# Performance work log

Measured on AMD Instinct MI355X. Metric: run time of the kernel, lower is better.

Reference implementation:

```python
import jax, jax.numpy as jnp
import numpy as np

D_MODEL = 256
N = 8192

def setup_inputs() -> dict:
    key = jax.random.key(0)
    k1, k2, k3, k4 = jax.random.split(key, 4)
    x = jax.random.normal(k1, (N, D_MODEL), dtype=jnp.float32)
    # nn.Linear weights: shape [out, in], applied as x @ W.T
    s = 1.0 / np.sqrt(D_MODEL)
    Wq = jax.random.normal(k2, (D_MODEL, D_MODEL), dtype=jnp.float32) * s
    Wk = jax.random.normal(k3, (D_MODEL, D_MODEL), dtype=jnp.float32) * s
    Wv = jax.random.normal(k4, (D_MODEL, D_MODEL), dtype=jnp.float32) * s
    return {"x": x, "Wq": Wq, "Wk": Wk, "Wv": Wv}

def reference(x, Wq, Wk, Wv):
    d_model = Wq.shape[0]
    Q = x @ Wq.T  # [N, d]
    K = x @ Wk.T
    V = x @ Wv.T
    scores = (Q @ K.T) / jnp.sqrt(jnp.asarray(d_model, x.dtype))  # [N, N]
    attn = jax.nn.softmax(scores, axis=-1)  # stable max-sub softmax, same math
    cntx = attn @ V  # [N, d]
    return (cntx, attn)
```

## Files before the change

kernel.cpp:

```cpp
#include <hip/hip_runtime.h>

#define D_MODEL 256
#define NSEQ    8192
#define PV_GROUPS 8

typedef _Float16 half8 __attribute__((ext_vector_type(8)));
typedef _Float16 half4 __attribute__((ext_vector_type(4)));
typedef float    f32x4 __attribute__((ext_vector_type(4)));

__device__ __forceinline__ half8 cvt8(f32x4 a, f32x4 b) {
  half8 h;
  h[0]=(_Float16)a[0]; h[1]=(_Float16)a[1]; h[2]=(_Float16)a[2]; h[3]=(_Float16)a[3];
  h[4]=(_Float16)b[0]; h[5]=(_Float16)b[1]; h[6]=(_Float16)b[2]; h[7]=(_Float16)b[3];
  return h;
}

__device__ __forceinline__ half8 load8_f32(const float* p) {
  f32x4 a = *(const f32x4*)p;
  f32x4 b = *(const f32x4*)(p + 4);
  return cvt8(a, b);
}

__global__ __launch_bounds__(64, 3) void qkv_kernel(
    const float* __restrict__ x, const float* __restrict__ Wq,
    const float* __restrict__ Wk, const float* __restrict__ Wv,
    _Float16* __restrict__ QK16, _Float16* __restrict__ VT)
{
  const int lane = threadIdx.x & 63;
  const int c    = lane & 15;
  const int quad = lane >> 4;
  const int M0   = blockIdx.x * 64;
  const int Nblk = blockIdx.y * 64;
  const int widx = Nblk >> 8;
  const int nloc = Nblk & 255;
  const float* W = (widx == 0) ? Wq : (widx == 1 ? Wk : Wv);

  f32x4 acc[4][4] = {};
  for (int k0 = 0; k0 < D_MODEL; k0 += 32) {
    half8 af[4], bf[4];
#pragma unroll
    for (int mt = 0; mt < 4; ++mt)
      af[mt] = load8_f32(&x[(size_t)(M0 + mt*16 + c) * D_MODEL + k0 + quad*8]);
#pragma unroll
    for (int nt = 0; nt < 4; ++nt)
      bf[nt] = load8_f32(&W[(size_t)(nloc + nt*16 + c) * D_MODEL + k0 + quad*8]);
#pragma unroll
    for (int mt = 0; mt < 4; ++mt)
#pragma unroll
      for (int nt = 0; nt < 4; ++nt)
        acc[mt][nt] = __builtin_amdgcn_mfma_f32_16x16x32_f16(af[mt], bf[nt], acc[mt][nt], 0, 0, 0);
  }

  if (widx < 2) {
#pragma unroll
    for (int mt = 0; mt < 4; ++mt)
#pragma unroll
      for (int nt = 0; nt < 4; ++nt) {
        const int col  = widx * 256 + nloc + nt*16 + c;
        const int row0 = M0 + mt*16 + quad*4;
#pragma unroll
        for (int r = 0; r < 4; ++r)
          QK16[(size_t)(row0 + r) * 512 + col] = (_Float16)acc[mt][nt][r];
      }
  } else {
#pragma unroll
    for (int mt = 0; mt < 4; ++mt)
#pragma unroll
      for (int nt = 0; nt < 4; ++nt) {
        const int d  = nloc + nt*16 + c;
        const int m0 = M0 + mt*16 + quad*4;
        half4 h;
        h[0]=(_Float16)acc[mt][nt][0]; h[1]=(_Float16)acc[mt][nt][1];
        h[2]=(_Float16)acc[mt][nt][2]; h[3]=(_Float16)acc[mt][nt][3];
        *(half4*)&VT[(size_t)d * NSEQ + m0] = h;
      }
  }
}

template<bool P16>
__global__ __launch_bounds__(256, 3) void score_kernel(
    const _Float16* __restrict__ QK16, void* __restrict__ Pout,
    float* __restrict__ lsum)
{
  const int tid  = threadIdx.x;
  const int lane = tid & 63;
  const int wave = tid >> 6;
  const int c    = lane & 15;
  const int quad = lane >> 4;
  const int M0   = blockIdx.x * 128 + (wave >> 1) * 64;
  const int N0   = blockIdx.y * 128 + (wave & 1) * 64;

  f32x4 acc[4][4] = {};
  half8 afA[4], bfA[4], afB[4], bfB[4];

  auto ld = [&](half8 (&af)[4], half8 (&bf)[4], int k0) {
#pragma unroll
    for (int mt = 0; mt < 4; ++mt)
      af[mt] = *(const half8*)&QK16[(size_t)(M0 + mt*16 + c) * 512 + k0 + quad*8];
#pragma unroll
    for (int nt = 0; nt < 4; ++nt)
      bf[nt] = *(const half8*)&QK16[(size_t)(N0 + nt*16 + c) * 512 + 256 + k0 + quad*8];
  };
  auto mm = [&](half8 (&af)[4], half8 (&bf)[4]) {
#pragma unroll
    for (int mt = 0; mt < 4; ++mt)
#pragma unroll
      for (int nt = 0; nt < 4; ++nt)
        acc[mt][nt] = __builtin_amdgcn_mfma_f32_16x16x32_f16(af[mt], bf[nt], acc[mt][nt], 0, 0, 0);
  };

  ld(afA, bfA, 0);
#pragma unroll
  for (int k0 = 0; k0 < 256; k0 += 64) {
    ld(afB, bfB, k0 + 32);
    mm(afA, bfA);
    if (k0 + 64 < 256) ld(afA, bfA, k0 + 64);
    mm(afB, bfB);
  }

  float psum[4][4] = {};
#pragma unroll
  for (int mt = 0; mt < 4; ++mt)
#pragma unroll
    for (int nt = 0; nt < 4; ++nt)
#pragma unroll
      for (int r = 0; r < 4; ++r) {
        const float p = __expf(acc[mt][nt][r] * 0.0625f);
        psum[mt][r] += p;
        const size_t idx = (size_t)(M0 + mt*16 + quad*4 + r) * NSEQ + N0 + nt*16 + c;
        if constexpr (P16) ((_Float16*)Pout)[idx] = (_Float16)p;
        else               ((float*)Pout)[idx]    = p;
      }

#pragma unroll
  for (int mt = 0; mt < 4; ++mt)
#pragma unroll
    for (int r = 0; r < 4; ++r) {
      float v = psum[mt][r];
      v += __shfl_xor(v, 1);
      v += __shfl_xor(v, 2);
      v += __shfl_xor(v, 4);
      v += __shfl_xor(v, 8);
      if (c == 0) atomicAdd(&lsum[M0 + mt*16 + quad*4 + r], v);
    }
}

__global__ __launch_bounds__(256, 3) void pv_kernel_p16(
    const _Float16* __restrict__ P16, float* __restrict__ attn,
    const float* __restrict__ lsum, const _Float16* __restrict__ VT,
    float* __restrict__ cntx)
{
  __shared__ float linv[32];
  const int tid  = threadIdx.x;
  const int lane = tid & 63;
  const int wave = tid >> 6;
  const int c    = lane & 15;
  const int quad = lane >> 4;
  const int M0   = blockIdx.x * 32;
  const int jb   = blockIdx.y * (NSEQ / PV_GROUPS);
  const int je   = jb + NSEQ / PV_GROUPS;
  const int D0   = wave * 64;
  const int nr   = tid >> 3;
  const int ncol = (tid & 7) * 8;

  if (tid < 32) linv[tid] = 1.0f / lsum[M0 + tid];
  __syncthreads();
  const float nscale = linv[nr];

  f32x4 acc[2][4] = {};
  half8 afA[2][2], bfA[4][2], npA;
  half8 afB[2][2], bfB[4][2], npB;

  auto ld = [&](half8 (&af)[2][2], half8 (&bf)[4][2], half8& np, int j0) {
    np = *(const half8*)&P16[(size_t)(M0 + nr) * NSEQ + j0 + ncol];
#pragma unroll
    for (int h = 0; h < 2; ++h) {
#pragma unroll
      for (int mt = 0; mt < 2; ++mt)
        af[mt][h] = *(const half8*)&P16[(size_t)(M0 + mt*16 + c) * NSEQ + j0 + h*32 + quad*8];
#pragma unroll
      for (int nt = 0; nt < 4; ++nt)
        bf[nt][h] = *(const half8*)&VT[(size_t)(D0 + nt*16 + c) * NSEQ + j0 + h*32 + quad*8];
    }
  };
  auto consume = [&](half8 (&af)[2][2], half8 (&bf)[4][2], half8& np, int j0) {
    f32x4 w0, w1;
#pragma unroll
    for (int r = 0; r < 4; ++r) {
      w0[r] = (float)np[r]     * nscale;
      w1[r] = (float)np[r + 4] * nscale;
    }
    float* ar = attn + (size_t)(M0 + nr) * NSEQ + j0 + ncol;
    *(f32x4*)ar       = w0;
    *(f32x4*)(ar + 4) = w1;
#pragma unroll
    for (int h = 0; h < 2; ++h)
#pragma unroll
      for (int mt = 0; mt < 2; ++mt)
#pragma unroll
        for (int nt = 0; nt < 4; ++nt)
          acc[mt][nt] = __builtin_amdgcn_mfma_f32_16x16x32_f16(af[mt][h], bf[nt][h], acc[mt][nt], 0, 0, 0);
  };

  ld(afA, bfA, npA, jb);
  for (int j0 = jb; j0 < je; j0 += 128) {
    ld(afB, bfB, npB, j0 + 64);
    consume(afA, bfA, npA, j0);
    if (j0 + 128 < je) ld(afA, bfA, npA, j0 + 128);
    consume(afB, bfB, npB, j0 + 64);
  }

#pragma unroll
  for (int mt = 0; mt < 2; ++mt)
#pragma unroll
    for (int r = 0; r < 4; ++r) {
      const float s = linv[mt*16 + quad*4 + r];
#pragma unroll
      for (int nt = 0; nt < 4; ++nt)
        atomicAdd(&cntx[(size_t)(M0 + mt*16 + quad*4 + r) * D_MODEL + D0 + nt*16 + c],
                  acc[mt][nt][r] * s);
    }
}

__global__ __launch_bounds__(256) void pv_kernel_f32(
    const float* __restrict__ Pin, float* __restrict__ attn,
    const float* __restrict__ lsum, const _Float16* __restrict__ VT,
    float* __restrict__ cntx)
{
  __shared__ float linv[32];
  const int tid  = threadIdx.x;
  const int lane = tid & 63;
  const int wave = tid >> 6;
  const int c    = lane & 15;
  const int quad = lane >> 4;
  const int M0   = blockIdx.x * 32;
  const int jb   = blockIdx.y * (NSEQ / PV_GROUPS);
  const int je   = jb + NSEQ / PV_GROUPS;
  const int D0   = wave * 64;
  const int nr   = tid >> 3;
  const int ncol = (tid & 7) * 8;

  if (tid < 32) linv[tid] = 1.0f / lsum[M0 + tid];
  __syncthreads();
  const float nscale = linv[nr];

  f32x4 acc[2][4] = {};
  for (int j0 = jb; j0 < je; j0 += 64) {
    const float* pr = Pin + (size_t)(M0 + nr) * NSEQ + j0 + ncol;
    f32x4 np0 = *(const f32x4*)pr;
    f32x4 np1 = *(const f32x4*)(pr + 4);

    half8 af[2][2], bf[4][2];
#pragma unroll
    for (int h = 0; h < 2; ++h) {
#pragma unroll
      for (int mt = 0; mt < 2; ++mt) {
        const float* pa = Pin + (size_t)(M0 + mt*16 + c) * NSEQ + j0 + h*32 + quad*8;
        af[mt][h] = cvt8(*(const f32x4*)pa, *(const f32x4*)(pa + 4));
      }
#pragma unroll
      for (int nt = 0; nt < 4; ++nt)
        bf[nt][h] = *(const half8*)&VT[(size_t)(D0 + nt*16 + c) * NSEQ + j0 + h*32 + quad*8];
    }

    __syncthreads();

    float* ar = attn + (size_t)(M0 + nr) * NSEQ + j0 + ncol;
    *(f32x4*)ar       = np0 * nscale;
    *(f32x4*)(ar + 4) = np1 * nscale;

#pragma unroll
    for (int h = 0; h < 2; ++h)
#pragma unroll
      for (int mt = 0; mt < 2; ++mt)
#pragma unroll
        for (int nt = 0; nt < 4; ++nt)
          acc[mt][nt] = __builtin_amdgcn_mfma_f32_16x16x32_f16(af[mt][h], bf[nt][h], acc[mt][nt], 0, 0, 0);
  }

#pragma unroll
  for (int mt = 0; mt < 2; ++mt)
#pragma unroll
    for (int r = 0; r < 4; ++r) {
      const float s = linv[mt*16 + quad*4 + r];
#pragma unroll
      for (int nt = 0; nt < 4; ++nt)
        atomicAdd(&cntx[(size_t)(M0 + mt*16 + quad*4 + r) * D_MODEL + D0 + nt*16 + c],
                  acc[mt][nt][r] * s);
    }
}

extern "C" void kernel_launch(void* const* d_in, const int* in_sizes, int n_in,
                              void* d_out, int out_size, void* d_ws, size_t ws_size,
                              hipStream_t stream)
{
  const float* x  = (const float*)d_in[0];
  const float* Wq = (const float*)d_in[1];
  const float* Wk = (const float*)d_in[2];
  const float* Wv = (const float*)d_in[3];

  float* cntx = (float*)d_out;
  float* attn = cntx + (size_t)NSEQ * D_MODEL;

  _Float16* QK16 = (_Float16*)d_ws;
  _Float16* VT   = QK16 + (size_t)NSEQ * 512;
  float*    lsum = (float*)(VT + (size_t)D_MODEL * NSEQ);
  _Float16* P16  = (_Float16*)(lsum + NSEQ);

  const size_t base_bytes = (size_t)NSEQ*512*2 + (size_t)D_MODEL*NSEQ*2 + (size_t)NSEQ*4;
  const bool big_ws = ws_size >= base_bytes + (size_t)NSEQ * NSEQ * 2;

  hipMemsetAsync(cntx, 0, sizeof(float) * (size_t)NSEQ * D_MODEL, stream);
  hipMemsetAsync(lsum, 0, sizeof(float) * NSEQ, stream);

  qkv_kernel<<<dim3(128, 12), 64, 0, stream>>>(x, Wq, Wk, Wv, QK16, VT);

  if (big_ws) {
    score_kernel<true><<<dim3(64, 64), 256, 0, stream>>>(QK16, (void*)P16, lsum);
    pv_kernel_p16<<<dim3(NSEQ/32, PV_GROUPS), 256, 0, stream>>>(P16, attn, lsum, VT, cntx);
  } else {
    score_kernel<false><<<dim3(64, 64), 256, 0, stream>>>(QK16, (void*)attn, lsum);
    pv_kernel_f32<<<dim3(NSEQ/32, PV_GROUPS), 256, 0, stream>>>(attn, attn, lsum, VT, cntx);
  }
}
```

Before: 642.2 us.

## Store fp16 probabilities in MFMA-fragment tiled layout and stage via LDS DMA

```diff
diff --git a/kernel.cpp b/kernel.cpp
--- a/kernel.cpp
+++ b/kernel.cpp
@@ -7,6 +7,9 @@
 typedef _Float16 half8 __attribute__((ext_vector_type(8)));
 typedef _Float16 half4 __attribute__((ext_vector_type(4)));
 typedef float    f32x4 __attribute__((ext_vector_type(4)));
+
+typedef __attribute__((address_space(1))) const void* gptr_t;
+typedef __attribute__((address_space(3))) void*       lptr_t;
 
 __device__ __forceinline__ half8 cvt8(f32x4 a, f32x4 b) {
   half8 h;
@@ -20,6 +23,7 @@
   f32x4 b = *(const f32x4*)(p + 4);
   return cvt8(a, b);
 }
+
 
 __global__ __launch_bounds__(64, 3) void qkv_kernel(
     const float* __restrict__ x, const float* __restrict__ Wq,
@@ -120,17 +124,26 @@
 
   float psum[4][4] = {};
 #pragma unroll
-  for (int mt = 0; mt < 4; ++mt)
-#pragma unroll
-    for (int nt = 0; nt < 4; ++nt)
+  for (int mt = 0; mt < 4; ++mt) {
+    const size_t tq = (size_t)((M0 + mt*16) >> 4);
+#pragma unroll
+    for (int nt = 0; nt < 4; ++nt) {
+      const size_t tj   = (size_t)((N0 >> 5) + (nt >> 1));
+      const size_t base = (tq * 256 + tj) * 512
+                        + (size_t)(((nt*2 + (c>>3)) & 3) * 128 + quad*32 + (c & 7));
 #pragma unroll
       for (int r = 0; r < 4; ++r) {
         const float p = __expf(acc[mt][nt][r] * 0.0625f);
         psum[mt][r] += p;
-        const size_t idx = (size_t)(M0 + mt*16 + quad*4 + r) * NSEQ + N0 + nt*16 + c;
-        if constexpr (P16) ((_Float16*)Pout)[idx] = (_Float16)p;
-        else               ((float*)Pout)[idx]    = p;
-      }
+        if constexpr (P16) {
+          ((_Float16*)Pout)[base + r*8] = (_Float16)p;
+        } else {
+          const size_t idx = (size_t)(M0 + mt*16 + quad*4 + r) * NSEQ + N0 + nt*16 + c;
+          ((float*)Pout)[idx] = p;
+        }
+      }
+    }
+  }
 
 #pragma unroll
   for (int mt = 0; mt < 4; ++mt)
@@ -145,8 +158,99 @@
     }
 }
 
-__global__ __launch_bounds__(256, 3) void pv_kernel_p16(
-    const _Float16* __restrict__ P16, float* __restrict__ attn,
+__global__ __launch_bounds__(256) void pv_kernel_p16(
+    const _Float16* __restrict__ P16F, float* __restrict__ attn,
+    const float* __restrict__ lsum, const _Float16* __restrict__ VT,
+    float* __restrict__ cntx)
+{
+  __shared__ alignas(16) _Float16 As[2 * 4 * 512];
+  __shared__ float linv[32];
+  const int tid  = threadIdx.x;
+  const int lane = tid & 63;
+  const int wave = tid >> 6;
+  const int c    = lane & 15;
+  const int quad = lane >> 4;
+  const int M0   = blockIdx.x * 32;
+  const int jb   = blockIdx.y * (NSEQ / PV_GROUPS);
+  const int je   = jb + NSEQ / PV_GROUPS;
+  const int D0   = wave * 64;
+  const int wmt  = wave >> 1;
+  const int wks  = wave & 1;
+
+  if (tid < 32) linv[tid] = 1.0f / lsum[M0 + tid];
+
+  const size_t tq = (size_t)((M0 >> 4) + wmt);
+
+  {
+    const _Float16* src = P16F + (tq * 256 + (size_t)((jb >> 5) + wks)) * 512 + lane * 8;
+    __builtin_amdgcn_global_load_lds((gptr_t)src, (lptr_t)&As[wave * 512], 16, 0, 0);
+  }
+  __syncthreads();
+
+  const float sw = linv[wmt * 16 + c];
+
+  f32x4 acc[2][4] = {};
+  int buf = 0;
+  for (int j0 = jb; j0 < je; j0 += 64) {
+    if (j0 + 64 < je) {
+      const _Float16* src = P16F + (tq * 256 + (size_t)(((j0 + 64) >> 5) + wks)) * 512 + lane * 8;
+      __builtin_amdgcn_global_load_lds((gptr_t)src,
+          (lptr_t)&As[(buf ^ 1) * 2048 + wave * 512], 16, 0, 0);
+    }
+
+    half8 af[2][2];
+#pragma unroll
+    for (int mt = 0; mt < 2; ++mt)
+#pragma unroll
+      for (int ks = 0; ks < 2; ++ks)
+        af[mt][ks] = *(const half8*)&As[buf * 2048 + (mt*2 + ks) * 512 + lane * 8];
+
+    half8 bf[4][2];
+#pragma unroll
+    for (int ks = 0; ks < 2; ++ks)
+#pragma unroll
+      for (int nt = 0; nt < 4; ++nt)
+        bf[nt][ks] = *(const half8*)&VT[(size_t)(D0 + nt*16 + c) * NSEQ + j0 + ks*32 + quad*8];
+
+    {
+      const half8 v = af[wmt][wks];
+      f32x4 w0, w1;
+#pragma unroll
+      for (int r = 0; r < 4; ++r) {
+        w0[r] = (float)v[r]     * sw;
+        w1[r] = (float)v[r + 4] * sw;
+      }
+      float* ar = attn + (size_t)(M0 + wmt*16 + c) * NSEQ + j0 + wks*32 + quad*8;
+      *(f32x4*)ar       = w0;
+      *(f32x4*)(ar + 4) = w1;
+    }
+
+#pragma unroll
+    for (int ks = 0; ks < 2; ++ks)
+#pragma unroll
+      for (int mt = 0; mt < 2; ++mt)
+#pragma unroll
+        for (int nt = 0; nt < 4; ++nt)
+          acc[mt][nt] = __builtin_amdgcn_mfma_f32_16x16x32_f16(af[mt][ks], bf[nt][ks], acc[mt][nt], 0, 0, 0);
+
+    __syncthreads();
+    buf ^= 1;
+  }
+
+#pragma unroll
+  for (int mt = 0; mt < 2; ++mt)
+#pragma unroll
+    for (int r = 0; r < 4; ++r) {
+      const float s = linv[mt*16 + quad*4 + r];
+#pragma unroll
+      for (int nt = 0; nt < 4; ++nt)
+        atomicAdd(&cntx[(size_t)(M0 + mt*16 + quad*4 + r) * D_MODEL + D0 + nt*16 + c],
+                  acc[mt][nt][r] * s);
+    }
+}
+
+__global__ __launch_bounds__(256) void pv_kernel_f32(
+    const float* __restrict__ Pin, float* __restrict__ attn,
     const float* __restrict__ lsum, const _Float16* __restrict__ VT,
     float* __restrict__ cntx)
 {
@@ -168,83 +272,6 @@
   const float nscale = linv[nr];
 
   f32x4 acc[2][4] = {};
-  half8 afA[2][2], bfA[4][2], npA;
-  half8 afB[2][2], bfB[4][2], npB;
-
-  auto ld = [&](half8 (&af)[2][2], half8 (&bf)[4][2], half8& np, int j0) {
-    np = *(const half8*)&P16[(size_t)(M0 + nr) * NSEQ + j0 + ncol];
-#pragma unroll
-    for (int h = 0; h < 2; ++h) {
-#pragma unroll
-      for (int mt = 0; mt < 2; ++mt)
-        af[mt][h] = *(const half8*)&P16[(size_t)(M0 + mt*16 + c) * NSEQ + j0 + h*32 + quad*8];
-#pragma unroll
-      for (int nt = 0; nt < 4; ++nt)
-        bf[nt][h] = *(const half8*)&VT[(size_t)(D0 + nt*16 + c) * NSEQ + j0 + h*32 + quad*8];
-    }
-  };
-  auto consume = [&](half8 (&af)[2][2], half8 (&bf)[4][2], half8& np, int j0) {
-    f32x4 w0, w1;
-#pragma unroll
-    for (int r = 0; r < 4; ++r) {
-      w0[r] = (float)np[r]     * nscale;
-      w1[r] = (float)np[r + 4] * nscale;
-    }
-    float* ar = attn + (size_t)(M0 + nr) * NSEQ + j0 + ncol;
-    *(f32x4*)ar       = w0;
-    *(f32x4*)(ar + 4) = w1;
-#pragma unroll
-    for (int h = 0; h < 2; ++h)
-#pragma unroll
-      for (int mt = 0; mt < 2; ++mt)
-#pragma unroll
-        for (int nt = 0; nt < 4; ++nt)
-          acc[mt][nt] = __builtin_amdgcn_mfma_f32_16x16x32_f16(af[mt][h], bf[nt][h], acc[mt][nt], 0, 0, 0);
-  };
-
-  ld(afA, bfA, npA, jb);
-  for (int j0 = jb; j0 < je; j0 += 128) {
-    ld(afB, bfB, npB, j0 + 64);
-    consume(afA, bfA, npA, j0);
-    if (j0 + 128 < je) ld(afA, bfA, npA, j0 + 128);
-    consume(afB, bfB, npB, j0 + 64);
-  }
-
-#pragma unroll
-  for (int mt = 0; mt < 2; ++mt)
-#pragma unroll
-    for (int r = 0; r < 4; ++r) {
-      const float s = linv[mt*16 + quad*4 + r];
-#pragma unroll
-      for (int nt = 0; nt < 4; ++nt)
-        atomicAdd(&cntx[(size_t)(M0 + mt*16 + quad*4 + r) * D_MODEL + D0 + nt*16 + c],
-                  acc[mt][nt][r] * s);
-    }
-}
-
-__global__ __launch_bounds__(256) void pv_kernel_f32(
-    const float* __restrict__ Pin, float* __restrict__ attn,
-    const float* __restrict__ lsum, const _Float16* __restrict__ VT,
-    float* __restrict__ cntx)
-{
-  __shared__ float linv[32];
-  const int tid  = threadIdx.x;
-  const int lane = tid & 63;
-  const int wave = tid >> 6;
-  const int c    = lane & 15;
-  const int quad = lane >> 4;
-  const int M0   = blockIdx.x * 32;
-  const int jb   = blockIdx.y * (NSEQ / PV_GROUPS);
-  const int je   = jb + NSEQ / PV_GROUPS;
-  const int D0   = wave * 64;
-  const int nr   = tid >> 3;
-  const int ncol = (tid & 7) * 8;
-
-  if (tid < 32) linv[tid] = 1.0f / lsum[M0 + tid];
-  __syncthreads();
-  const float nscale = linv[nr];
-
-  f32x4 acc[2][4] = {};
   for (int j0 = jb; j0 < je; j0 += 64) {
     const float* pr = Pin + (size_t)(M0 + nr) * NSEQ + j0 + ncol;
     f32x4 np0 = *(const f32x4*)pr;
@@ -305,7 +332,7 @@
   _Float16* QK16 = (_Float16*)d_ws;
   _Float16* VT   = QK16 + (size_t)NSEQ * 512;
   float*    lsum = (float*)(VT + (size_t)D_MODEL * NSEQ);
-  _Float16* P16  = (_Float16*)(lsum + NSEQ);
+  _Float16* P16F = (_Float16*)(lsum + NSEQ);
 
   const size_t base_bytes = (size_t)NSEQ*512*2 + (size_t)D_MODEL*NSEQ*2 + (size_t)NSEQ*4;
   const bool big_ws = ws_size >= base_bytes + (size_t)NSEQ * NSEQ * 2;
@@ -316,8 +343,8 @@
   qkv_kernel<<<dim3(128, 12), 64, 0, stream>>>(x, Wq, Wk, Wv, QK16, VT);
 
   if (big_ws) {
-    score_kernel<true><<<dim3(64, 64), 256, 0, stream>>>(QK16, (void*)P16, lsum);
-    pv_kernel_p16<<<dim3(NSEQ/32, PV_GROUPS), 256, 0, stream>>>(P16, attn, lsum, VT, cntx);
+    score_kernel<true><<<dim3(64, 64), 256, 0, stream>>>(QK16, (void*)P16F, lsum);
+    pv_kernel_p16<<<dim3(NSEQ/32, PV_GROUPS), 256, 0, stream>>>(P16F, attn, lsum, VT, cntx);
   } else {
     score_kernel<false><<<dim3(64, 64), 256, 0, stream>>>(QK16, (void*)attn, lsum);
     pv_kernel_f32<<<dim3(NSEQ/32, PV_GROUPS), 256, 0, stream>>>(attn, attn, lsum, VT, cntx);
```

Result: slower. 696.1 us (+8.4%).
